# Performance work log

Measured on AMD Instinct MI355X. Metric: run time of the kernel, lower is better.

The kernel has to match this reference:

```python
import jax, jax.numpy as jnp
import numpy as np

N_NODES = 50000
N_EDGES = 800000
N_GRAPHS = 128
IN_CH = 16
IN_CTX = 16
H_G = 128
H_C = 128
H_F = 128


def _lin_init(key, fan_in, fan_out):
    k1, k2 = jax.random.split(key)
    s = 1.0 / np.sqrt(fan_in)
    W = jax.random.uniform(k1, (fan_in, fan_out), minval=-s, maxval=s, dtype=jnp.float32)
    b = jax.random.uniform(k2, (fan_out,), minval=-s, maxval=s, dtype=jnp.float32)
    return W, b


def setup_inputs() -> dict:
    key = jax.random.key(0)
    ks = jax.random.split(key, 16)
    inp = {}
    inp['x'] = jax.random.normal(ks[0], (N_NODES, IN_CH), dtype=jnp.float32)
    inp['x_context'] = jax.random.normal(ks[1], (N_GRAPHS, IN_CTX), dtype=jnp.float32)
    inp['edge_index'] = jax.random.randint(ks[2], (2, N_EDGES), 0, N_NODES, dtype=jnp.int64)
    inp['batch'] = jnp.sort(jax.random.randint(ks[3], (N_NODES,), 0, N_GRAPHS, dtype=jnp.int64))
    inp['edge_weight'] = jax.random.uniform(ks[4], (N_EDGES,), dtype=jnp.float32)
    # graph conv weights (GCNConv): layer0 [IN_CH,H_G], layers1-3 [H_G,H_G]
    dims = [(IN_CH, H_G), (H_G, H_G), (H_G, H_G), (H_G, H_G)]
    for i, (di, do) in enumerate(dims):
        W, b = _lin_init(ks[5 + i], di, do)
        inp[f'gW{i}'] = W
        inp[f'gb{i}'] = b
    # context FC: [IN_CTX,H_C], [H_C,H_C], [H_C,H_C]
    cdims = [(IN_CTX, H_C), (H_C, H_C), (H_C, H_C)]
    for i, (di, do) in enumerate(cdims):
        W, b = _lin_init(ks[9 + i], di, do)
        inp[f'cW{i}'] = W
        inp[f'cb{i}'] = b
    # fc stack: [H_G+H_C,H_F], [H_F,H_F], [H_F,H_F]
    fdims = [(H_G + H_C, H_F), (H_F, H_F), (H_F, H_F)]
    for i, (di, do) in enumerate(fdims):
        W, b = _lin_init(ks[12 + i], di, do)
        inp[f'fW{i}'] = W
        inp[f'fb{i}'] = b
    return inp


def _forward(x, x_context, edge_index, batch, edge_weight,
             gWs, gbs, cWs, cbs, fWs, fbs):
    n = x.shape[0]
    src, dst = edge_index[0], edge_index[1]
    loop = jnp.arange(n, dtype=edge_index.dtype)
    # GCN: add self-loops with weight 1, symmetric normalization
    src_f = jnp.concatenate([src, loop])
    dst_f = jnp.concatenate([dst, loop])
    ew_f = jnp.concatenate([edge_weight, jnp.ones((n,), dtype=edge_weight.dtype)])
    deg = jax.ops.segment_sum(ew_f, dst_f, num_segments=n)
    dinv = jnp.where(deg > 0, jax.lax.rsqrt(jnp.where(deg > 0, deg, 1.0)), 0.0)
    norm = dinv[src_f] * ew_f * dinv[dst_f]  # [E+N]

    h = x
    for W, b in zip(gWs, gbs):
        hw = h @ W                                   # [N, H_G]
        msg = norm[:, None] * hw[src_f]              # gather + scale
        h = jax.ops.segment_sum(msg, dst_f, num_segments=n) + b
        h = jax.nn.relu(h)

    # global mean pool over graphs
    s = jax.ops.segment_sum(h, batch, num_segments=N_GRAPHS)
    cnt = jax.ops.segment_sum(jnp.ones((n,), dtype=h.dtype), batch, num_segments=N_GRAPHS)
    g = s / jnp.maximum(cnt, 1.0)[:, None]           # [G, H_G]

    c = x_context
    for W, b in zip(cWs, cbs):
        c = jax.nn.relu(c @ W + b)

    z = jnp.concatenate([g, c], axis=-1)             # [G, H_G + H_C]
    for W, b in zip(fWs[:-1], fbs[:-1]):
        z = jax.nn.relu(z @ W + b)
    z = z @ fWs[-1] + fbs[-1]
    return z


def reference(x, x_context, edge_index, batch, edge_weight,
              gW0, gb0, gW1, gb1, gW2, gb2, gW3, gb3,
              cW0, cb0, cW1, cb1, cW2, cb2,
              fW0, fb0, fW1, fb1, fW2, fb2):
    return _forward(x, x_context, edge_index, batch, edge_weight,
                    [gW0, gW1, gW2, gW3], [gb0, gb1, gb2, gb3],
                    [cW0, cW1, cW2], [cb0, cb1, cb2],
                    [fW0, fW1, fW2], [fb0, fb1, fb2])
```

## Files before the change

### kernel.cpp

```cpp
#include <hip/hip_runtime.h>

typedef __attribute__((ext_vector_type(8))) short short8;
typedef __attribute__((ext_vector_type(4))) float f32x4;

#define IN_CH 16
#define CAP 64

__device__ inline unsigned int bf16_rne(float f) {
  unsigned int u = __float_as_uint(f);
  unsigned int r = u + 0x7fffu + ((u >> 16) & 1u);
  return r >> 16;
}
__device__ inline float bf16lo(unsigned int g) { return __uint_as_float(g << 16); }
__device__ inline float bf16hi(unsigned int g) { return __uint_as_float(g & 0xffff0000u); }
__device__ inline short8 as_short8(uint4 u) {
  union { uint4 u; short8 s; } cv; cv.u = u; return cv.s;
}

__global__ void zero_kernel(int* __restrict__ cnt, int n) {
  int i = blockIdx.x * blockDim.x + threadIdx.x;
  for (int j = i; j < n; j += gridDim.x * blockDim.x) cnt[j] = 0;
}

__global__ void build_kernel(const int* __restrict__ ei, const float* __restrict__ ew,
                             int* __restrict__ cnt, int2* __restrict__ bucket, int E) {
  int e = blockIdx.x * blockDim.x + threadIdx.x;
  if (e < E) {
    int dst = ei[E + e];
    int old = atomicAdd(&cnt[dst], 1);
    if (old < CAP) {
      int2 p;
      p.x = ei[e];
      p.y = __float_as_int(ew[e]);
      bucket[(size_t)dst * CAP + old] = p;
    }
  }
}

__global__ __launch_bounds__(256) void node_prep_kernel(
    const int* __restrict__ cnt, const int2* __restrict__ bucket,
    const float* __restrict__ x, float* __restrict__ dinv,
    float* __restrict__ xs, int n) {
  int lane = threadIdx.x & 15;
  int v = blockIdx.x * 16 + (threadIdx.x >> 4);
  if (v >= n) return;
  int c = min(cnt[v], CAP);
  float s = 0.f;
  for (int j = lane; j < c; j += 16)
    s += __int_as_float(bucket[(size_t)v * CAP + j].y);
#pragma unroll
  for (int off = 1; off < 16; off <<= 1) s += __shfl_xor(s, off);
  float dv = rsqrtf(1.0f + s);
  if (lane == 0) dinv[v] = dv;
  xs[(size_t)v * 16 + lane] = dv * x[(size_t)v * 16 + lane];
}

__global__ __launch_bounds__(256) void spmm16_kernel(
    const float4* __restrict__ xs4, const float* __restrict__ dinv,
    const int* __restrict__ cnt, const int2* __restrict__ bucket,
    float4* __restrict__ A0_4, int n) {
  const int l = threadIdx.x & 63;
  const int q = l >> 2;
  const int c4 = l & 3;
  const int v = (blockIdx.x << 2) + (threadIdx.x >> 6);
  if (v >= n) return;
  const size_t beg = (size_t)v * CAP;
  const int c = min(cnt[v], CAP);
  float4 s = make_float4(0.f, 0.f, 0.f, 0.f);
  for (int j = 0; j < c; j += 16) {
    int jj = j + q;
    bool ok = jj < c;
    int2 p = bucket[ok ? beg + jj : beg];
    float w = ok ? __int_as_float(p.y) : 0.f;
    float4 u = xs4[(size_t)p.x * 4 + c4];
    s.x += w * u.x; s.y += w * u.y; s.z += w * u.z; s.w += w * u.w;
  }
#pragma unroll
  for (int off = 4; off < 64; off <<= 1) {
    s.x += __shfl_xor(s.x, off);
    s.y += __shfl_xor(s.y, off);
    s.z += __shfl_xor(s.z, off);
    s.w += __shfl_xor(s.w, off);
  }
  float dv = dinv[v];
  float4 self = xs4[(size_t)v * 4 + c4];
  if (q == 0) {
    float4 o;
    o.x = dv * (s.x + self.x);
    o.y = dv * (s.y + self.y);
    o.z = dv * (s.z + self.z);
    o.w = dv * (s.w + self.w);
    A0_4[(size_t)v * 4 + c4] = o;
  }
}

__global__ __launch_bounds__(256) void spmm_bf16_kernel(
    const uint4* __restrict__ Hs4, const float* __restrict__ dinv,
    const int* __restrict__ cnt, const int2* __restrict__ bucket,
    uint4* __restrict__ Ab4, int n) {
  const int l = threadIdx.x & 63;
  const int q = l >> 4;
  const int c16 = l & 15;
  const int v = (blockIdx.x << 2) + (threadIdx.x >> 6);
  if (v >= n) return;
  const size_t beg = (size_t)v * CAP;
  const int c = min(cnt[v], CAP);
  float s[8] = {};
  for (int j = 0; j < c; j += 16) {
#pragma unroll
    for (int i = 0; i < 4; ++i) {
      int jj = j + i * 4 + q;
      bool ok = jj < c;
      int2 p = bucket[ok ? beg + jj : beg];
      float w = ok ? __int_as_float(p.y) : 0.f;
      uint4 u = Hs4[(size_t)p.x * 16 + c16];
      s[0] += w * bf16lo(u.x); s[1] += w * bf16hi(u.x);
      s[2] += w * bf16lo(u.y); s[3] += w * bf16hi(u.y);
      s[4] += w * bf16lo(u.z); s[5] += w * bf16hi(u.z);
      s[6] += w * bf16lo(u.w); s[7] += w * bf16hi(u.w);
    }
  }
#pragma unroll
  for (int j = 0; j < 8; ++j) {
    s[j] += __shfl_xor(s[j], 16);
    s[j] += __shfl_xor(s[j], 32);
  }
  float dv = dinv[v];
  uint4 self = Hs4[(size_t)v * 16 + c16];
  float r0 = dv * (s[0] + bf16lo(self.x));
  float r1 = dv * (s[1] + bf16hi(self.x));
  float r2 = dv * (s[2] + bf16lo(self.y));
  float r3 = dv * (s[3] + bf16hi(self.y));
  float r4 = dv * (s[4] + bf16lo(self.z));
  float r5 = dv * (s[5] + bf16hi(self.z));
  float r6 = dv * (s[6] + bf16lo(self.w));
  float r7 = dv * (s[7] + bf16hi(self.w));
  if (q == 0) {
    uint4 o;
    o.x = bf16_rne(r0) | (bf16_rne(r1) << 16);
    o.y = bf16_rne(r2) | (bf16_rne(r3) << 16);
    o.z = bf16_rne(r4) | (bf16_rne(r5) << 16);
    o.w = bf16_rne(r6) | (bf16_rne(r7) << 16);
    Ab4[(size_t)v * 16 + c16] = o;
  }
}

__global__ __launch_bounds__(256) void gemm16_kernel(
    const float* __restrict__ X, const float* __restrict__ W,
    const float* __restrict__ bias, const float* __restrict__ dinv,
    unsigned int* __restrict__ Hb, int n) {
  __shared__ float Ws[16][128];
  __shared__ float Xs[32][16];
  const int tid = threadIdx.x;
  const int row0 = blockIdx.x * 32;

  for (int i = tid * 4; i < 16 * 128; i += 1024)
    *(float4*)&Ws[0][i] = *(const float4*)&W[i];
  for (int i = tid * 4; i < 32 * 16; i += 1024) {
    int r = i / 16, k = i % 16;
    int rr = row0 + r;
    float4 v = make_float4(0.f, 0.f, 0.f, 0.f);
    if (rr < n) v = *(const float4*)&X[(size_t)rr * 16 + k];
    *(float4*)&Xs[r][k] = v;
  }
  __syncthreads();

  const int tc = (tid & 31) * 4;
  const int tr = (tid >> 5) * 4;
  float acc[4][4] = {};
  for (int k = 0; k < 16; k += 4) {
    float4 xv[4];
#pragma unroll
    for (int r = 0; r < 4; ++r) xv[r] = *(const float4*)&Xs[tr + r][k];
    float4 wv[4];
#pragma unroll
    for (int kk = 0; kk < 4; ++kk) wv[kk] = *(const float4*)&Ws[k + kk][tc];
#pragma unroll
    for (int r = 0; r < 4; ++r) {
      float xr[4] = {xv[r].x, xv[r].y, xv[r].z, xv[r].w};
#pragma unroll
      for (int kk = 0; kk < 4; ++kk) {
        acc[r][0] += xr[kk] * wv[kk].x;
        acc[r][1] += xr[kk] * wv[kk].y;
        acc[r][2] += xr[kk] * wv[kk].z;
        acc[r][3] += xr[kk] * wv[kk].w;
      }
    }
  }

  float4 bv = *(const float4*)&bias[tc];
#pragma unroll
  for (int r = 0; r < 4; ++r) {
    int rr = row0 + tr + r;
    if (rr < n) {
      float dv = dinv[rr];
      float o0 = dv * fmaxf(acc[r][0] + bv.x, 0.f);
      float o1 = dv * fmaxf(acc[r][1] + bv.y, 0.f);
      float o2 = dv * fmaxf(acc[r][2] + bv.z, 0.f);
      float o3 = dv * fmaxf(acc[r][3] + bv.w, 0.f);
      uint2 st;
      st.x = bf16_rne(o0) | (bf16_rne(o1) << 16);
      st.y = bf16_rne(o2) | (bf16_rne(o3) << 16);
      *(uint2*)&Hb[(size_t)rr * 64 + (tc >> 1)] = st;
    }
  }
}

__global__ void prep_wt3_kernel(const float* __restrict__ W1, const float* __restrict__ W2,
                                const float* __restrict__ W3, unsigned int* __restrict__ Wt) {
  int gid = blockIdx.x * 256 + threadIdx.x;
  if (gid >= 3 * 128 * 64) return;
  int layer = gid >> 13;
  int idx = gid & 8191;
  const float* W = (layer == 0) ? W1 : (layer == 1) ? W2 : W3;
  int c = idx >> 6, kp = idx & 63;
  float f0 = W[(2 * kp) * 128 + c];
  float f1 = W[(2 * kp + 1) * 128 + c];
  Wt[gid] = bf16_rne(f0) | (bf16_rne(f1) << 16);
}

#define TOFF1 2048
#define TOFF2 (TOFF1 + 16384)
#define TOFF3 (TOFF2 + 16384)
#define TOFF4 (TOFF3 + 32768)
#define TOFF5 (TOFF4 + 16384)
#define TTOTAL (TOFF5 + 16384)
__global__ void prep_tail_kernel(
    const float* __restrict__ cW0, const float* __restrict__ cW1, const float* __restrict__ cW2,
    const float* __restrict__ fW0, const float* __restrict__ fW1, const float* __restrict__ fW2,
    float* __restrict__ WT) {
  int gid = blockIdx.x * 256 + threadIdx.x;
  if (gid >= TTOTAL) return;
  const float* W; int lgK, idx;
  if (gid < TOFF1)      { W = cW0; lgK = 4; idx = gid; }
  else if (gid < TOFF2) { W = cW1; lgK = 7; idx = gid - TOFF1; }
  else if (gid < TOFF3) { W = cW2; lgK = 7; idx = gid - TOFF2; }
  else if (gid < TOFF4) { W = fW0; lgK = 8; idx = gid - TOFF3; }
  else if (gid < TOFF5) { W = fW1; lgK = 7; idx = gid - TOFF4; }
  else                  { W = fW2; lgK = 7; idx = gid - TOFF5; }
  int c = idx >> lgK, k = idx & ((1 << lgK) - 1);
  WT[gid] = W[k * 128 + c];
}

__global__ __launch_bounds__(256) void gemm_mfma_kernel(
    const unsigned int* __restrict__ Ab, const unsigned int* __restrict__ Wtb,
    const float* __restrict__ bias, const float* __restrict__ dinv, int scale_out,
    unsigned short* __restrict__ Hh, int n) {
  __shared__ unsigned int Wlds[128 * 68];
  const int tid = threadIdx.x;
  for (int idx = tid; idx < 128 * 16; idx += 256) {
    int row = idx >> 4, slot = idx & 15;
    uint4 v = ((const uint4*)Wtb)[idx];
    *(uint4*)&Wlds[row * 68 + slot * 4] = v;
  }
  __syncthreads();

  const int lane = tid & 63, wid = tid >> 6;
  const int r0 = blockIdx.x * 128 + wid * 32;
  const int rowA = r0 + (lane & 15);
  const int kgrp = lane >> 4;
  const uint4* Abase = (const uint4*)Ab;

  f32x4 acc[2][8] = {};
#pragma unroll
  for (int kstep = 0; kstep < 4; ++kstep) {
    short8 a[2];
#pragma unroll
    for (int rb = 0; rb < 2; ++rb)
      a[rb] = as_short8(Abase[(size_t)(rowA + rb * 16) * 16 + kstep * 4 + kgrp]);
#pragma unroll
    for (int cb = 0; cb < 8; ++cb) {
      short8 b = as_short8(*(const uint4*)&Wlds[(cb * 16 + (lane & 15)) * 68 + (kstep * 4 + kgrp) * 4]);
      acc[0][cb] = __builtin_amdgcn_mfma_f32_16x16x32_bf16(a[0], b, acc[0][cb], 0, 0, 0);
      acc[1][cb] = __builtin_amdgcn_mfma_f32_16x16x32_bf16(a[1], b, acc[1][cb], 0, 0, 0);
    }
  }

  const int rbase = kgrp * 4;
  float dsc[2][4];
#pragma unroll
  for (int rb = 0; rb < 2; ++rb)
#pragma unroll
    for (int i = 0; i < 4; ++i) {
      int row = r0 + rb * 16 + rbase + i;
      dsc[rb][i] = (scale_out && row < n) ? dinv[row] : 1.0f;
    }

#pragma unroll
  for (int cb = 0; cb < 8; ++cb) {
    int col = cb * 16 + (lane & 15);
    float bv = bias[col];
#pragma unroll
    for (int rb = 0; rb < 2; ++rb) {
#pragma unroll
      for (int i = 0; i < 4; ++i) {
        int row = r0 + rb * 16 + rbase + i;
        if (row < n) {
          float o = dsc[rb][i] * fmaxf(acc[rb][cb][i] + bv, 0.f);
          Hh[(size_t)row * 128 + col] = (unsigned short)bf16_rne(o);
        }
      }
    }
  }
}

__global__ __launch_bounds__(256) void pool_part_kernel(
    const unsigned int* __restrict__ Hb, const int* __restrict__ batch,
    float* __restrict__ gpp, int G, int n) {
  int b = blockIdx.x;
  int g = b >> 2, chunk = b & 3;
  int lo = 0, hi = n;
  while (lo < hi) { int mid = (lo + hi) >> 1; if (batch[mid] < g) lo = mid + 1; else hi = mid; }
  int start = lo;
  lo = start; hi = n;
  while (lo < hi) { int mid = (lo + hi) >> 1; if (batch[mid] < g + 1) lo = mid + 1; else hi = mid; }
  int end = lo;

  int lane = threadIdx.x & 63, grp = threadIdx.x >> 6;
  float s0 = 0.f, s1 = 0.f;
  for (int v = start + chunk * 4 + grp; v < end; v += 16) {
    unsigned int u = Hb[((size_t)v << 6) + lane];
    s0 += bf16lo(u);
    s1 += bf16hi(u);
  }
  __shared__ float red[4][128];
  red[grp][2 * lane] = s0;
  red[grp][2 * lane + 1] = s1;
  __syncthreads();
  if (threadIdx.x < 128) {
    float t = red[0][threadIdx.x] + red[1][threadIdx.x] + red[2][threadIdx.x] + red[3][threadIdx.x];
    gpp[((size_t)chunk * G + g) * 128 + threadIdx.x] = t;
  }
}

__device__ inline void tlayer(const float* __restrict__ WTl, const float* __restrict__ bg,
                              const float* in_lds, float* out_lds,
                              float (*psum)[128], int K, int tid, int relu_,
                              float* __restrict__ gout) {
  const int c = tid & 127, kh = tid >> 7;
  const int kcnt = K >> 1;
  const float4* w4 = (const float4*)(WTl + (size_t)c * K + kh * kcnt);
  const float4* i4 = (const float4*)(in_lds + kh * kcnt);
  const int n4 = kcnt >> 2;
  __syncthreads();
  float acc = 0.f;
#pragma unroll 8
  for (int t = 0; t < n4; ++t) {
    float4 wv = w4[t];
    float4 iv = i4[t];
    acc += iv.x * wv.x + iv.y * wv.y + iv.z * wv.z + iv.w * wv.w;
  }
  psum[kh][c] = acc;
  __syncthreads();
  if (tid < 128) {
    float r = psum[0][c] + psum[1][c] + bg[c];
    if (relu_) r = fmaxf(r, 0.f);
    if (gout) gout[c] = r; else out_lds[c] = r;
  }
}

__global__ __launch_bounds__(256) void tail2_kernel(
    const float* __restrict__ gpp, const int* __restrict__ batch,
    const float* __restrict__ xc, const float* __restrict__ WT,
    const float* __restrict__ cb0, const float* __restrict__ cb1, const float* __restrict__ cb2,
    const float* __restrict__ fb0, const float* __restrict__ fb1, const float* __restrict__ fb2,
    float* __restrict__ out, int G, int n) {
  __shared__ float z[256];
  __shared__ float tA[128];
  __shared__ float tB[128];
  __shared__ float xin[16];
  __shared__ float psum[2][128];
  __shared__ float invc_sh;

  const int g = blockIdx.x;
  const int tid = threadIdx.x;

  if (tid < 128) {
    float t = gpp[((size_t)0 * G + g) * 128 + tid] + gpp[((size_t)1 * G + g) * 128 + tid] +
              gpp[((size_t)2 * G + g) * 128 + tid] + gpp[((size_t)3 * G + g) * 128 + tid];
    z[tid] = t;
  } else if (tid < 144) {
    xin[tid - 128] = xc[g * 16 + (tid - 128)];
  } else if (tid == 144) {
    int lo = 0, hi = n;
    while (lo < hi) { int m = (lo + hi) >> 1; if (batch[m] < g) lo = m + 1; else hi = m; }
    int st = lo;
    lo = st; hi = n;
    while (lo < hi) { int m = (lo + hi) >> 1; if (batch[m] < g + 1) lo = m + 1; else hi = m; }
    invc_sh = 1.0f / fmaxf((float)(lo - st), 1.0f);
  }
  __syncthreads();
  if (tid < 128) z[tid] *= invc_sh;

  tlayer(WT,          cb0, xin, tA,      psum, 16,  tid, 1, nullptr);
  tlayer(WT + TOFF1,  cb1, tA,  tB,      psum, 128, tid, 1, nullptr);
  tlayer(WT + TOFF2,  cb2, tB,  z + 128, psum, 128, tid, 1, nullptr);
  tlayer(WT + TOFF3,  fb0, z,   tA,      psum, 256, tid, 1, nullptr);
  tlayer(WT + TOFF4,  fb1, tA,  tB,      psum, 128, tid, 1, nullptr);
  tlayer(WT + TOFF5,  fb2, tB,  nullptr, psum, 128, tid, 0, out + (size_t)g * 128);
}

extern "C" void kernel_launch(void* const* d_in, const int* in_sizes, int n_in,
                              void* d_out, int out_size, void* d_ws, size_t ws_size,
                              hipStream_t stream) {
  const float* x     = (const float*)d_in[0];
  const float* xc    = (const float*)d_in[1];
  const int*   ei    = (const int*)d_in[2];
  const int*   batch = (const int*)d_in[3];
  const float* ew    = (const float*)d_in[4];
  const float* gW[4] = {(const float*)d_in[5], (const float*)d_in[7], (const float*)d_in[9],  (const float*)d_in[11]};
  const float* gb[4] = {(const float*)d_in[6], (const float*)d_in[8], (const float*)d_in[10], (const float*)d_in[12]};
  const float* cW0 = (const float*)d_in[13]; const float* cb0 = (const float*)d_in[14];
  const float* cW1 = (const float*)d_in[15]; const float* cb1 = (const float*)d_in[16];
  const float* cW2 = (const float*)d_in[17]; const float* cb2 = (const float*)d_in[18];
  const float* fW0 = (const float*)d_in[19]; const float* fb0 = (const float*)d_in[20];
  const float* fW1 = (const float*)d_in[21]; const float* fb1 = (const float*)d_in[22];
  const float* fW2 = (const float*)d_in[23]; const float* fb2 = (const float*)d_in[24];
  float* out = (float*)d_out;

  const int N = in_sizes[3];
  const int E = in_sizes[4];
  const int G = in_sizes[1] / IN_CH;
  const int Np = (N + 127) & ~127;

  char* p = (char*)d_ws;
  auto alloc = [&](size_t bytes) { char* r = p; p += (bytes + 255) & ~(size_t)255; return r; };
  int*   cnt    = (int*)  alloc((size_t)N * 4);
  int2*  bucket = (int2*) alloc((size_t)N * CAP * 8);
  float* dinv   = (float*)alloc((size_t)N * 4);
  float* xs     = (float*)alloc((size_t)N * 16 * 4);
  float* A0     = (float*)alloc((size_t)N * 16 * 4);
  unsigned int* Ab = (unsigned int*)alloc((size_t)Np * 64 * 4);
  unsigned int* Hb = (unsigned int*)alloc((size_t)Np * 64 * 4);
  unsigned int* Wt = (unsigned int*)alloc((size_t)3 * 128 * 64 * 4);
  float* WT  = (float*)alloc((size_t)TTOTAL * 4);
  float* gpp = (float*)alloc((size_t)4 * G * 128 * 4);

  int nbE = (E + 255) / 256;

  zero_kernel<<<128, 256, 0, stream>>>(cnt, N);
  build_kernel<<<nbE, 256, 0, stream>>>(ei, ew, cnt, bucket, E);
  node_prep_kernel<<<(N + 15) / 16, 256, 0, stream>>>(cnt, bucket, x, dinv, xs, N);

  prep_wt3_kernel<<<96, 256, 0, stream>>>(gW[1], gW[2], gW[3], Wt);
  prep_tail_kernel<<<(TTOTAL + 255) / 256, 256, 0, stream>>>(cW0, cW1, cW2, fW0, fW1, fW2, WT);

  spmm16_kernel<<<(N + 3) / 4, 256, 0, stream>>>((const float4*)xs, dinv, cnt, bucket,
                                                 (float4*)A0, N);
  gemm16_kernel<<<(N + 31) / 32, 256, 0, stream>>>(A0, gW[0], gb[0], dinv, Hb, N);

  for (int l = 0; l < 3; ++l) {
    spmm_bf16_kernel<<<(N + 3) / 4, 256, 0, stream>>>((const uint4*)Hb, dinv, cnt, bucket,
                                                      (uint4*)Ab, N);
    gemm_mfma_kernel<<<Np / 128, 256, 0, stream>>>(Ab, Wt + (size_t)l * 8192, gb[l + 1], dinv,
                                                   (l < 2) ? 1 : 0, (unsigned short*)Hb, N);
  }

  pool_part_kernel<<<4 * G, 256, 0, stream>>>(Hb, batch, gpp, G, N);
  tail2_kernel<<<G, 256, 0, stream>>>(gpp, batch, xc, WT, cb0, cb1, cb2,
                                      fb0, fb1, fb2, out, G, N);
}
```

Before: 285.5 us.

## Fuse layer-0 SpMM with its GEMM and merge prep/zero kernels

Merges the zeroing of the count array and the two weight-transpose prep kernels into one grid-stride kernel, removing two launches. Fuses the 16-channel layer-0 aggregation into the layer-0 GEMM, so aggregated rows go straight to shared memory instead of through a global A0 buffer. The cost is that each block now handles 32 nodes with only 4 waves doing the gather serially over 8 passes, which may lower latency hiding for the irregular gather.

New measurement: 300.5 us. 5.3% more time.

```diff
diff --git a/kernel.cpp b/kernel.cpp
--- a/kernel.cpp
+++ b/kernel.cpp
@@ -17,9 +17,46 @@
   union { uint4 u; short8 s; } cv; cv.u = u; return cv.s;
 }
 
-__global__ void zero_kernel(int* __restrict__ cnt, int n) {
-  int i = blockIdx.x * blockDim.x + threadIdx.x;
-  for (int j = i; j < n; j += gridDim.x * blockDim.x) cnt[j] = 0;
+#define TOFF1 2048
+#define TOFF2 (TOFF1 + 16384)
+#define TOFF3 (TOFF2 + 16384)
+#define TOFF4 (TOFF3 + 32768)
+#define TOFF5 (TOFF4 + 16384)
+#define TTOTAL (TOFF5 + 16384)
+#define WT3CNT (3 * 128 * 64)
+
+__global__ void prep_all_kernel(
+    const float* __restrict__ W1, const float* __restrict__ W2, const float* __restrict__ W3,
+    unsigned int* __restrict__ Wt,
+    const float* __restrict__ cW0, const float* __restrict__ cW1, const float* __restrict__ cW2,
+    const float* __restrict__ fW0, const float* __restrict__ fW1, const float* __restrict__ fW2,
+    float* __restrict__ WT, int* __restrict__ cnt, int n) {
+  int gid = blockIdx.x * 256 + threadIdx.x;
+  int total = WT3CNT + TTOTAL + n;
+  for (int i = gid; i < total; i += gridDim.x * 256) {
+    if (i < WT3CNT) {
+      int layer = i >> 13;
+      int idx = i & 8191;
+      const float* W = (layer == 0) ? W1 : (layer == 1) ? W2 : W3;
+      int c = idx >> 6, kp = idx & 63;
+      float f0 = W[(2 * kp) * 128 + c];
+      float f1 = W[(2 * kp + 1) * 128 + c];
+      Wt[i] = bf16_rne(f0) | (bf16_rne(f1) << 16);
+    } else if (i < WT3CNT + TTOTAL) {
+      int g = i - WT3CNT;
+      const float* W; int lgK, idx;
+      if (g < TOFF1)      { W = cW0; lgK = 4; idx = g; }
+      else if (g < TOFF2) { W = cW1; lgK = 7; idx = g - TOFF1; }
+      else if (g < TOFF3) { W = cW2; lgK = 7; idx = g - TOFF2; }
+      else if (g < TOFF4) { W = fW0; lgK = 8; idx = g - TOFF3; }
+      else if (g < TOFF5) { W = fW1; lgK = 7; idx = g - TOFF4; }
+      else                { W = fW2; lgK = 7; idx = g - TOFF5; }
+      int c = idx >> lgK, k = idx & ((1 << lgK) - 1);
+      WT[g] = W[k * 128 + c];
+    } else {
+      cnt[i - WT3CNT - TTOTAL] = 0;
+    }
+  }
 }
 
 __global__ void build_kernel(const int* __restrict__ ei, const float* __restrict__ ew,
@@ -55,42 +92,99 @@
   xs[(size_t)v * 16 + lane] = dv * x[(size_t)v * 16 + lane];
 }
 
-__global__ __launch_bounds__(256) void spmm16_kernel(
+__global__ __launch_bounds__(256) void layer0_kernel(
     const float4* __restrict__ xs4, const float* __restrict__ dinv,
     const int* __restrict__ cnt, const int2* __restrict__ bucket,
-    float4* __restrict__ A0_4, int n) {
-  const int l = threadIdx.x & 63;
+    const float* __restrict__ W, const float* __restrict__ bias,
+    unsigned int* __restrict__ Hb, int n) {
+  __shared__ float Ws[16][128];
+  __shared__ float Xs[32][16];
+  const int tid = threadIdx.x;
+  const int row0 = blockIdx.x * 32;
+
+  for (int i = tid * 4; i < 16 * 128; i += 1024)
+    *(float4*)&Ws[0][i] = *(const float4*)&W[i];
+
+  const int l = tid & 63;
+  const int wv = tid >> 6;
   const int q = l >> 2;
   const int c4 = l & 3;
-  const int v = (blockIdx.x << 2) + (threadIdx.x >> 6);
-  if (v >= n) return;
-  const size_t beg = (size_t)v * CAP;
-  const int c = min(cnt[v], CAP);
-  float4 s = make_float4(0.f, 0.f, 0.f, 0.f);
-  for (int j = 0; j < c; j += 16) {
-    int jj = j + q;
-    bool ok = jj < c;
-    int2 p = bucket[ok ? beg + jj : beg];
-    float w = ok ? __int_as_float(p.y) : 0.f;
-    float4 u = xs4[(size_t)p.x * 4 + c4];
-    s.x += w * u.x; s.y += w * u.y; s.z += w * u.z; s.w += w * u.w;
-  }
-#pragma unroll
-  for (int off = 4; off < 64; off <<= 1) {
-    s.x += __shfl_xor(s.x, off);
-    s.y += __shfl_xor(s.y, off);
-    s.z += __shfl_xor(s.z, off);
-    s.w += __shfl_xor(s.w, off);
-  }
-  float dv = dinv[v];
-  float4 self = xs4[(size_t)v * 4 + c4];
-  if (q == 0) {
-    float4 o;
-    o.x = dv * (s.x + self.x);
-    o.y = dv * (s.y + self.y);
-    o.z = dv * (s.z + self.z);
-    o.w = dv * (s.w + self.w);
-    A0_4[(size_t)v * 4 + c4] = o;
+#pragma unroll
+  for (int pass = 0; pass < 8; ++pass) {
+    int r = pass * 4 + wv;
+    int v = row0 + r;
+    if (v < n) {
+      size_t beg = (size_t)v * CAP;
+      int c = min(cnt[v], CAP);
+      float4 s = make_float4(0.f, 0.f, 0.f, 0.f);
+      for (int j = 0; j < c; j += 16) {
+        int jj = j + q;
+        bool ok = jj < c;
+        int2 p = bucket[ok ? beg + jj : beg];
+        float w = ok ? __int_as_float(p.y) : 0.f;
+        float4 u = xs4[(size_t)p.x * 4 + c4];
+        s.x += w * u.x; s.y += w * u.y; s.z += w * u.z; s.w += w * u.w;
+      }
+#pragma unroll
+      for (int off = 4; off < 64; off <<= 1) {
+        s.x += __shfl_xor(s.x, off);
+        s.y += __shfl_xor(s.y, off);
+        s.z += __shfl_xor(s.z, off);
+        s.w += __shfl_xor(s.w, off);
+      }
+      if (q == 0) {
+        float dv = dinv[v];
+        float4 self = xs4[(size_t)v * 4 + c4];
+        Xs[r][c4 * 4 + 0] = dv * (s.x + self.x);
+        Xs[r][c4 * 4 + 1] = dv * (s.y + self.y);
+        Xs[r][c4 * 4 + 2] = dv * (s.z + self.z);
+        Xs[r][c4 * 4 + 3] = dv * (s.w + self.w);
+      }
+    } else if (q == 0) {
+      Xs[r][c4 * 4 + 0] = 0.f; Xs[r][c4 * 4 + 1] = 0.f;
+      Xs[r][c4 * 4 + 2] = 0.f; Xs[r][c4 * 4 + 3] = 0.f;
+    }
+  }
+  __syncthreads();
+
+  const int tc = (tid & 31) * 4;
+  const int tr = (tid >> 5) * 4;
+  float acc[4][4] = {};
+  for (int k = 0; k < 16; k += 4) {
+    float4 xv[4];
+#pragma unroll
+    for (int r = 0; r < 4; ++r) xv[r] = *(const float4*)&Xs[tr + r][k];
+    float4 wv4[4];
+#pragma unroll
+    for (int kk = 0; kk < 4; ++kk) wv4[kk] = *(const float4*)&Ws[k + kk][tc];
+#pragma unroll
+    for (int r = 0; r < 4; ++r) {
+      float xr[4] = {xv[r].x, xv[r].y, xv[r].z, xv[r].w};
+#pragma unroll
+      for (int kk = 0; kk < 4; ++kk) {
+        acc[r][0] += xr[kk] * wv4[kk].x;
+        acc[r][1] += xr[kk] * wv4[kk].y;
+        acc[r][2] += xr[kk] * wv4[kk].z;
+        acc[r][3] += xr[kk] * wv4[kk].w;
+      }
+    }
+  }
+
+  float4 bv = *(const float4*)&bias[tc];
+#pragma unroll
+  for (int r = 0; r < 4; ++r) {
+    int rr = row0 + tr + r;
+    if (rr < n) {
+      float dv = dinv[rr];
+      float o0 = dv * fmaxf(acc[r][0] + bv.x, 0.f);
+      float o1 = dv * fmaxf(acc[r][1] + bv.y, 0.f);
+      float o2 = dv * fmaxf(acc[r][2] + bv.z, 0.f);
+      float o3 = dv * fmaxf(acc[r][3] + bv.w, 0.f);
+      uint2 st;
+      st.x = bf16_rne(o0) | (bf16_rne(o1) << 16);
+      st.y = bf16_rne(o2) | (bf16_rne(o3) << 16);
+      *(uint2*)&Hb[(size_t)rr * 64 + (tc >> 1)] = st;
+    }
   }
 }
 
@@ -145,103 +239,6 @@
   }
 }
 
-__global__ __launch_bounds__(256) void gemm16_kernel(
-    const float* __restrict__ X, const float* __restrict__ W,
-    const float* __restrict__ bias, const float* __restrict__ dinv,
-    unsigned int* __restrict__ Hb, int n) {
-  __shared__ float Ws[16][128];
-  __shared__ float Xs[32][16];
-  const int tid = threadIdx.x;
-  const int row0 = blockIdx.x * 32;
-
-  for (int i = tid * 4; i < 16 * 128; i += 1024)
-    *(float4*)&Ws[0][i] = *(const float4*)&W[i];
-  for (int i = tid * 4; i < 32 * 16; i += 1024) {
-    int r = i / 16, k = i % 16;
-    int rr = row0 + r;
-    float4 v = make_float4(0.f, 0.f, 0.f, 0.f);
-    if (rr < n) v = *(const float4*)&X[(size_t)rr * 16 + k];
-    *(float4*)&Xs[r][k] = v;
-  }
-  __syncthreads();
-
-  const int tc = (tid & 31) * 4;
-  const int tr = (tid >> 5) * 4;
-  float acc[4][4] = {};
-  for (int k = 0; k < 16; k += 4) {
-    float4 xv[4];
-#pragma unroll
-    for (int r = 0; r < 4; ++r) xv[r] = *(const float4*)&Xs[tr + r][k];
-    float4 wv[4];
-#pragma unroll
-    for (int kk = 0; kk < 4; ++kk) wv[kk] = *(const float4*)&Ws[k + kk][tc];
-#pragma unroll
-    for (int r = 0; r < 4; ++r) {
-      float xr[4] = {xv[r].x, xv[r].y, xv[r].z, xv[r].w};
-#pragma unroll
-      for (int kk = 0; kk < 4; ++kk) {
-        acc[r][0] += xr[kk] * wv[kk].x;
-        acc[r][1] += xr[kk] * wv[kk].y;
-        acc[r][2] += xr[kk] * wv[kk].z;
-        acc[r][3] += xr[kk] * wv[kk].w;
-      }
-    }
-  }
-
-  float4 bv = *(const float4*)&bias[tc];
-#pragma unroll
-  for (int r = 0; r < 4; ++r) {
-    int rr = row0 + tr + r;
-    if (rr < n) {
-      float dv = dinv[rr];
-      float o0 = dv * fmaxf(acc[r][0] + bv.x, 0.f);
-      float o1 = dv * fmaxf(acc[r][1] + bv.y, 0.f);
-      float o2 = dv * fmaxf(acc[r][2] + bv.z, 0.f);
-      float o3 = dv * fmaxf(acc[r][3] + bv.w, 0.f);
-      uint2 st;
-      st.x = bf16_rne(o0) | (bf16_rne(o1) << 16);
-      st.y = bf16_rne(o2) | (bf16_rne(o3) << 16);
-      *(uint2*)&Hb[(size_t)rr * 64 + (tc >> 1)] = st;
-    }
-  }
-}
-
-__global__ void prep_wt3_kernel(const float* __restrict__ W1, const float* __restrict__ W2,
-                                const float* __restrict__ W3, unsigned int* __restrict__ Wt) {
-  int gid = blockIdx.x * 256 + threadIdx.x;
-  if (gid >= 3 * 128 * 64) return;
-  int layer = gid >> 13;
-  int idx = gid & 8191;
-  const float* W = (layer == 0) ? W1 : (layer == 1) ? W2 : W3;
-  int c = idx >> 6, kp = idx & 63;
-  float f0 = W[(2 * kp) * 128 + c];
-  float f1 = W[(2 * kp + 1) * 128 + c];
-  Wt[gid] = bf16_rne(f0) | (bf16_rne(f1) << 16);
-}
-
-#define TOFF1 2048
-#define TOFF2 (TOFF1 + 16384)
-#define TOFF3 (TOFF2 + 16384)
-#define TOFF4 (TOFF3 + 32768)
-#define TOFF5 (TOFF4 + 16384)
-#define TTOTAL (TOFF5 + 16384)
-__global__ void prep_tail_kernel(
-    const float* __restrict__ cW0, const float* __restrict__ cW1, const float* __restrict__ cW2,
-    const float* __restrict__ fW0, const float* __restrict__ fW1, const float* __restrict__ fW2,
-    float* __restrict__ WT) {
-  int gid = blockIdx.x * 256 + threadIdx.x;
-  if (gid >= TTOTAL) return;
-  const float* W; int lgK, idx;
-  if (gid < TOFF1)      { W = cW0; lgK = 4; idx = gid; }
-  else if (gid < TOFF2) { W = cW1; lgK = 7; idx = gid - TOFF1; }
-  else if (gid < TOFF3) { W = cW2; lgK = 7; idx = gid - TOFF2; }
-  else if (gid < TOFF4) { W = fW0; lgK = 8; idx = gid - TOFF3; }
-  else if (gid < TOFF5) { W = fW1; lgK = 7; idx = gid - TOFF4; }
-  else                  { W = fW2; lgK = 7; idx = gid - TOFF5; }
-  int c = idx >> lgK, k = idx & ((1 << lgK) - 1);
-  WT[gid] = W[k * 128 + c];
-}
-
 __global__ __launch_bounds__(256) void gemm_mfma_kernel(
     const unsigned int* __restrict__ Ab, const unsigned int* __restrict__ Wtb,
     const float* __restrict__ bias, const float* __restrict__ dinv, int scale_out,
@@ -429,25 +426,21 @@
   int2*  bucket = (int2*) alloc((size_t)N * CAP * 8);
   float* dinv   = (float*)alloc((size_t)N * 4);
   float* xs     = (float*)alloc((size_t)N * 16 * 4);
-  float* A0     = (float*)alloc((size_t)N * 16 * 4);
   unsigned int* Ab = (unsigned int*)alloc((size_t)Np * 64 * 4);
   unsigned int* Hb = (unsigned int*)alloc((size_t)Np * 64 * 4);
-  unsigned int* Wt = (unsigned int*)alloc((size_t)3 * 128 * 64 * 4);
+  unsigned int* Wt = (unsigned int*)alloc((size_t)WT3CNT * 4);
   float* WT  = (float*)alloc((size_t)TTOTAL * 4);
   float* gpp = (float*)alloc((size_t)4 * G * 128 * 4);
 
   int nbE = (E + 255) / 256;
 
-  zero_kernel<<<128, 256, 0, stream>>>(cnt, N);
+  prep_all_kernel<<<512, 256, 0, stream>>>(gW[1], gW[2], gW[3], Wt,
+                                           cW0, cW1, cW2, fW0, fW1, fW2, WT, cnt, N);
   build_kernel<<<nbE, 256, 0, stream>>>(ei, ew, cnt, bucket, E);
   node_prep_kernel<<<(N + 15) / 16, 256, 0, stream>>>(cnt, bucket, x, dinv, xs, N);
 
-  prep_wt3_kernel<<<96, 256, 0, stream>>>(gW[1], gW[2], gW[3], Wt);
-  prep_tail_kernel<<<(TTOTAL + 255) / 256, 256, 0, stream>>>(cW0, cW1, cW2, fW0, fW1, fW2, WT);
-
-  spmm16_kernel<<<(N + 3) / 4, 256, 0, stream>>>((const float4*)xs, dinv, cnt, bucket,
-                                                 (float4*)A0, N);
-  gemm16_kernel<<<(N + 31) / 32, 256, 0, stream>>>(A0, gW[0], gb[0], dinv, Hb, N);
+  layer0_kernel<<<(N + 31) / 32, 256, 0, stream>>>((const float4*)xs, dinv, cnt, bucket,
+                                                   gW[0], gb[0], Hb, N);
 
   for (int l = 0; l < 3; ++l) {
     spmm_bf16_kernel<<<(N + 3) / 4, 256, 0, stream>>>((const uint4*)Hb, dinv, cnt, bucket,
```
